# Optimization experiments

Measured on AMD Instinct MI355X. Metric: run time of the kernel, lower is better.

The kernel has to match this reference:

```python
import jax, jax.numpy as jnp
import numpy as np

N_HEAD = 16

def setup_inputs() -> dict:
    key = jax.random.key(0)
    k1, k2, k3, k4 = jax.random.split(key, 4)
    B, S, D = 4, 1024, 1024
    x = jax.random.normal(k1, (B, S, D), dtype=jnp.float32)
    # 0/1 float mask: cls_mask[:,0] overrides row 0, cls_mask[:,1] overrides col 0
    cls_mask = jax.random.randint(k2, (B, 2, S), 0, 2).astype(jnp.float32)
    w_attn = jax.random.normal(k3, (D, 3 * D), dtype=jnp.float32) * 0.02
    b_attn = jnp.zeros((3 * D,), dtype=jnp.float32)
    w_proj = jax.random.normal(k4, (D, D), dtype=jnp.float32) * 0.02
    b_proj = jnp.zeros((D,), dtype=jnp.float32)
    return {"x": x, "cls_mask": cls_mask, "w_attn": w_attn, "b_attn": b_attn,
            "w_proj": w_proj, "b_proj": b_proj}

def reference(x, cls_mask, w_attn, b_attn, w_proj, b_proj):
    B, S, D = x.shape
    H = N_HEAD
    hd = D // H
    cm = jnp.broadcast_to(jnp.tril(jnp.ones((S, S), x.dtype))[None, None], (B, 1, S, S))
    cm = cm.at[:, :, 0, :].set(cls_mask[:, 0][:, None, :])
    cm = cm.at[:, :, :, 0].set(cls_mask[:, 1][:, None, :])
    qkv = x @ w_attn + b_attn                      # [B,S,3D]
    q, k, v = jnp.split(qkv, 3, axis=-1)
    split_heads = lambda t: t.reshape(B, S, H, hd).transpose(0, 2, 1, 3)  # [B,H,S,hd]
    q, k, v = split_heads(q), split_heads(k), split_heads(v)
    w = jnp.einsum('bhqd,bhkd->bhqk', q, k) / jnp.sqrt(jnp.asarray(hd, x.dtype))
    w = w * cm - 10000.0 * (1.0 - cm)
    w = jax.nn.softmax(w, axis=-1)
    a = jnp.einsum('bhqk,bhkd->bhqd', w, v)
    a = a.transpose(0, 2, 1, 3).reshape(B, S, D)   # merge heads
    a = a @ w_proj + b_proj
    present = jnp.stack((k, v))                    # [2,B,H,S,hd]
    return a, present
```

## Files before the change

### kernel.cpp

```cpp
#include <hip/hip_runtime.h>
#include <hip/hip_bf16.h>

typedef __bf16 bf16x8 __attribute__((ext_vector_type(8)));
typedef float f32x4 __attribute__((ext_vector_type(4)));

__device__ __forceinline__ f32x4 mfma16(bf16x8 a, bf16x8 b, f32x4 c) {
    return __builtin_amdgcn_mfma_f32_16x16x32_bf16(a, b, c, 0, 0, 0);
}

typedef __attribute__((address_space(1))) const unsigned int GUInt;
typedef __attribute__((address_space(3))) unsigned int LUInt;
__device__ __forceinline__ void gl_lds16(const void* g, void* l) {
    __builtin_amdgcn_global_load_lds((GUInt*)g, (LUInt*)l, 16, 0, 0);
}

__device__ __forceinline__ int psw(int row, int bir) {
    return row * 128 + (bir ^ ((row & 7) << 4));
}

__global__ __launch_bounds__(256) void prep_kernel(
    const float* __restrict__ x, __hip_bfloat16* __restrict__ Xbf,
    const float* __restrict__ w_attn, __hip_bfloat16* __restrict__ WattnT,
    const float* __restrict__ w_proj, __hip_bfloat16* __restrict__ WprojT) {
    __shared__ float tile[64][65];
    const int bid = blockIdx.x;
    const int tid = threadIdx.x;
    if (bid < 4096) {
        int i = bid * 256 + tid;
        float4 v = reinterpret_cast<const float4*>(x)[i];
        __hip_bfloat16 o[4];
        o[0] = __float2bfloat16(v.x); o[1] = __float2bfloat16(v.y);
        o[2] = __float2bfloat16(v.z); o[3] = __float2bfloat16(v.w);
        *reinterpret_cast<uint2*>(&Xbf[i * 4]) = *reinterpret_cast<const uint2*>(o);
        return;
    }
    const float* in; __hip_bfloat16* out; int K, N, t;
    if (bid < 4096 + 768) { t = bid - 4096; in = w_attn; out = WattnT; K = 1024; N = 3072; }
    else                  { t = bid - 4864; in = w_proj; out = WprojT; K = 1024; N = 1024; }
    const int kt = t & 15, nt = t >> 4;
    const int c = tid & 63, r4 = tid >> 6;
#pragma unroll
    for (int i = 0; i < 16; ++i) {
        int r = i * 4 + r4;
        tile[r][c] = in[(size_t)(kt * 64 + r) * N + nt * 64 + c];
    }
    __syncthreads();
#pragma unroll
    for (int i = 0; i < 16; ++i) {
        int rr = i * 4 + r4;
        out[(size_t)(nt * 64 + rr) * K + kt * 64 + c] = __float2bfloat16(tile[c][rr]);
    }
}

template <int EPI>
__global__ __launch_bounds__(256) void gemm_kernel(
    const __hip_bfloat16* __restrict__ A, const __hip_bfloat16* __restrict__ Bt,
    const float* __restrict__ bias, int M, int N, int K,
    float* __restrict__ Cf,
    __hip_bfloat16* __restrict__ Qbf, __hip_bfloat16* __restrict__ Kbf,
    __hip_bfloat16* __restrict__ VbfT, float* __restrict__ present) {
    __shared__ __align__(16) char As[128 * 128];
    __shared__ __align__(16) char Bs[128 * 128];
    const int tid = threadIdx.x;
    const int lane = tid & 63;
    const int w = tid >> 6;
    const int lr = lane & 15;
    const int lg = lane >> 4;
    const int wm = (w >> 1) * 64;
    const int wn = (w & 1) * 64;
    const int bm = blockIdx.y, bn = blockIdx.x;
    const int swz = (lr & 7) << 4;

    const int srow = tid >> 3;
    const int ccs = ((tid & 7) * 16) ^ ((srow & 7) << 4);
    const char* aBase = (const char*)A + ((size_t)(bm * 128 + srow) * K) * 2 + ccs;
    const char* bBase = (const char*)Bt + ((size_t)(bn * 128 + srow) * K) * 2 + ccs;

    f32x4 zv = {0.f, 0.f, 0.f, 0.f};
    f32x4 acc[4][4];
#pragma unroll
    for (int i = 0; i < 4; ++i)
#pragma unroll
        for (int j = 0; j < 4; ++j) acc[i][j] = zv;

    for (int k0 = 0; k0 < K; k0 += 64) {
#pragma unroll
        for (int j = 0; j < 4; ++j) {
            gl_lds16(aBase + ((size_t)j * 32 * K + k0) * 2, &As[j * 4096 + tid * 16]);
            gl_lds16(bBase + ((size_t)j * 32 * K + k0) * 2, &Bs[j * 4096 + tid * 16]);
        }
        __syncthreads();
#pragma unroll
        for (int kk = 0; kk < 2; ++kk) {
            bf16x8 af[4], bfr[4];
#pragma unroll
            for (int mt = 0; mt < 4; ++mt)
                af[mt] = *reinterpret_cast<const bf16x8*>(
                    &As[(wm + mt * 16 + lr) * 128 + ((kk * 64 + lg * 16) ^ swz)]);
#pragma unroll
            for (int nt = 0; nt < 4; ++nt)
                bfr[nt] = *reinterpret_cast<const bf16x8*>(
                    &Bs[(wn + nt * 16 + lr) * 128 + ((kk * 64 + lg * 16) ^ swz)]);
#pragma unroll
            for (int mt = 0; mt < 4; ++mt)
#pragma unroll
                for (int nt = 0; nt < 4; ++nt)
                    acc[mt][nt] = mfma16(af[mt], bfr[nt], acc[mt][nt]);
        }
        __syncthreads();
    }

#pragma unroll
    for (int mt = 0; mt < 4; ++mt) {
        const int mbase = bm * 128 + wm + mt * 16 + lg * 4;
        const int bb = mbase >> 10, s0 = mbase & 1023;
#pragma unroll
        for (int nt = 0; nt < 4; ++nt) {
            const int n = bn * 128 + wn + nt * 16 + lr;
            const float bias_n = bias[n];
            float v[4];
#pragma unroll
            for (int r = 0; r < 4; ++r) v[r] = acc[mt][nt][r] + bias_n;
            if (EPI == 0) {
#pragma unroll
                for (int r = 0; r < 4; ++r) Cf[(size_t)(mbase + r) * N + n] = v[r];
            } else {
                const int sec = n >> 10, nn = n & 1023;
                const int hh = nn >> 6, d = nn & 63;
                const int rowbase = ((bb * 16 + hh) * 1024 + s0) * 64 + d;
                if (sec == 0) {
#pragma unroll
                    for (int r = 0; r < 4; ++r) Qbf[rowbase + r * 64] = __float2bfloat16(v[r]);
                } else if (sec == 1) {
#pragma unroll
                    for (int r = 0; r < 4; ++r) {
                        Kbf[rowbase + r * 64] = __float2bfloat16(v[r]);
                        present[rowbase + r * 64] = v[r];
                    }
                } else {
                    __hip_bfloat16 pk[4];
#pragma unroll
                    for (int r = 0; r < 4; ++r) {
                        pk[r] = __float2bfloat16(v[r]);
                        present[4194304 + rowbase + r * 64] = v[r];
                    }
                    *reinterpret_cast<uint2*>(&VbfT[((bb * 16 + hh) * 64 + d) * 1024 + s0]) =
                        *reinterpret_cast<const uint2*>(pk);
                }
            }
        }
    }
}

template <bool FIRST>
__device__ __forceinline__ void attn_tile(
    const char* Kb, const char* Vb, int kv0, char* Pw,
    const bf16x8* aq, const float* clscol, const float* cls, int b, int qbase,
    f32x4* acc_o, f32x4& acc_l,
    int lr, int lg, int lk, int swz, bf16x8 ones, float SC) {
    f32x4 zv = {0.f, 0.f, 0.f, 0.f};
    f32x4 sacc[4];
#pragma unroll
    for (int nt = 0; nt < 4; ++nt) {
        const char* kr = Kb + (nt * 16 + lr) * 128;
        bf16x8 k0 = *reinterpret_cast<const bf16x8*>(kr + ((lg * 16) ^ swz));
        bf16x8 k1 = *reinterpret_cast<const bf16x8*>(kr + ((64 + lg * 16) ^ swz));
        sacc[nt] = mfma16(aq[1], k1, mfma16(aq[0], k0, zv));
    }
    float p[4][4];
#pragma unroll
    for (int nt = 0; nt < 4; ++nt) {
        int k_j = kv0 + nt * 16 + lr;
#pragma unroll
        for (int r = 0; r < 4; ++r) {
            int q_i = qbase + lg * 4 + r;
            float e = __builtin_amdgcn_exp2f(sacc[nt][r] * SC);
            p[nt][r] = (k_j <= q_i) ? e : 0.f;
        }
    }
    if (qbase == 0) {
#pragma unroll
        for (int nt = 0; nt < 4; ++nt) {
            float cr = cls[b * 2048 + kv0 + nt * 16 + lr];
            float e0 = __builtin_amdgcn_exp2f(sacc[nt][0] * SC);
            float pr = (cr != 0.f) ? e0 : 0.f;
            if (lg == 0) p[nt][0] = pr;
        }
    }
    if (FIRST) {
#pragma unroll
        for (int r = 0; r < 4; ++r) {
            float ec = __builtin_amdgcn_exp2f(sacc[0][r] * SC);
            float pc = (clscol[r] != 0.f) ? ec : 0.f;
            if (lr == 0) p[0][r] = pc;
        }
    }
#pragma unroll
    for (int nt = 0; nt < 4; ++nt)
#pragma unroll
        for (int r = 0; r < 4; ++r)
            *reinterpret_cast<__hip_bfloat16*>(&Pw[psw(lg * 4 + r, nt * 32 + lr * 2)]) =
                __float2bfloat16(p[nt][r]);
    bf16x8 pa0 = *reinterpret_cast<const bf16x8*>(&Pw[psw(lr, lk * 2)]);
    bf16x8 pa1 = *reinterpret_cast<const bf16x8*>(&Pw[psw(lr, 64 + lk * 2)]);
    acc_l = mfma16(pa1, ones, mfma16(pa0, ones, acc_l));
#pragma unroll
    for (int ntd = 0; ntd < 4; ++ntd) {
        const char* vr = Vb + (ntd * 16 + lr) * 128;
        bf16x8 v0 = *reinterpret_cast<const bf16x8*>(vr + ((lg * 16) ^ swz));
        bf16x8 v1 = *reinterpret_cast<const bf16x8*>(vr + ((64 + lg * 16) ^ swz));
        acc_o[ntd] = mfma16(pa1, v1, mfma16(pa0, v0, acc_o[ntd]));
    }
}

__global__ __launch_bounds__(256) void attn_kernel(
    const __hip_bfloat16* __restrict__ Qbf, const __hip_bfloat16* __restrict__ Kbf,
    const __hip_bfloat16* __restrict__ VbfT, const float* __restrict__ cls,
    __hip_bfloat16* __restrict__ Abf) {
    __shared__ __align__(16) char KV0[16384];
    __shared__ __align__(16) char KV1[16384];
    __shared__ __align__(16) char P_lds[4 * 2048];
    const int tid = threadIdx.x;
    const int lane = tid & 63;
    const int w = tid >> 6;
    const int lr = lane & 15;
    const int lg = lane >> 4;
    const int lk = lg * 8;
    const int bh = blockIdx.x;
    const int qx = blockIdx.y;
    const int b = bh >> 4, h = bh & 15;
    const int desc[16] = {15, 0, 14, 13, 12, 11, 10, 9, 8, 7, 6, 5, 4, 3, 2, 1};
    const int base = (qx + ((b & 2) ? 8 : 0)) & 15;
    const int pos = (b & 1) ? (15 - base) : base;
    const int qt = desc[pos];
    const int qbase = qt * 64 + w * 16;
    char* Pw = &P_lds[w * 2048];
    const int ntiles = (qt == 0) ? 16 : (qt + 1);

    const char* kSrc = (const char*)Kbf + (size_t)bh * 131072;
    const char* vSrc = (const char*)VbfT + (size_t)bh * 131072;
    const int srow = tid >> 3;
    const int ccs = ((tid & 7) * 16) ^ ((srow & 7) << 4);

#define STAGE(BUFPTR, T)                                                         \
    do {                                                                         \
        const int kv0s_ = (T) * 64;                                              \
        char* dst_ = &(BUFPTR)[tid * 16];                                        \
        gl_lds16(kSrc + (size_t)(kv0s_ + srow) * 128 + ccs, dst_);               \
        gl_lds16(kSrc + (size_t)(kv0s_ + 32 + srow) * 128 + ccs, dst_ + 4096);   \
        gl_lds16(vSrc + (size_t)srow * 2048 + kv0s_ * 2 + ccs, dst_ + 8192);     \
        gl_lds16(vSrc + (size_t)(32 + srow) * 2048 + kv0s_ * 2 + ccs, dst_ + 12288); \
    } while (0)

    STAGE(KV0, 0);

    bf16x8 aq[2];
#pragma unroll
    for (int c = 0; c < 2; ++c)
        aq[c] = *reinterpret_cast<const bf16x8*>(&Qbf[(size_t)(bh * 1024 + qbase + lr) * 64 + c * 32 + lk]);

    float clscol[4];
#pragma unroll
    for (int r = 0; r < 4; ++r)
        clscol[r] = cls[b * 2048 + 1024 + qbase + lg * 4 + r];

    bf16x8 ones;
#pragma unroll
    for (int i = 0; i < 8; ++i) ones[i] = (__bf16)1.0f;

    const float SC = 0.125f * 1.44269504088896f;
    f32x4 zv = {0.f, 0.f, 0.f, 0.f};
    f32x4 acc_o[4];
    f32x4 acc_l = zv;
#pragma unroll
    for (int i = 0; i < 4; ++i) acc_o[i] = zv;

    const int swz = (lr & 7) << 4;
    __syncthreads();

    STAGE(KV1, 1);
    attn_tile<true>(KV0, KV0 + 8192, 0, Pw, aq, clscol, cls, b, qbase,
                    acc_o, acc_l, lr, lg, lk, swz, ones, SC);
    __syncthreads();
    int t = 1;
    while (t < ntiles) {
        if (t + 1 < ntiles) STAGE(KV0, t + 1);
        attn_tile<false>(KV1, KV1 + 8192, t * 64, Pw, aq, clscol, cls, b, qbase,
                         acc_o, acc_l, lr, lg, lk, swz, ones, SC);
        __syncthreads();
        ++t;
        if (t >= ntiles) break;
        if (t + 1 < ntiles) STAGE(KV1, t + 1);
        attn_tile<false>(KV0, KV0 + 8192, t * 64, Pw, aq, clscol, cls, b, qbase,
                         acc_o, acc_l, lr, lg, lk, swz, ones, SC);
        __syncthreads();
        ++t;
    }
#undef STAGE

#pragma unroll
    for (int r = 0; r < 4; ++r) {
        float inv = 1.f / acc_l[r];
        int q_i = qbase + lg * 4 + r;
#pragma unroll
        for (int ntd = 0; ntd < 4; ++ntd) {
            int dd = ntd * 16 + lr;
            Abf[(size_t)(b * 1024 + q_i) * 1024 + h * 64 + dd] = __float2bfloat16(acc_o[ntd][r] * inv);
        }
    }
}

extern "C" void kernel_launch(void* const* d_in, const int* in_sizes, int n_in,
                              void* d_out, int out_size, void* d_ws, size_t ws_size,
                              hipStream_t stream) {
    const float* x      = (const float*)d_in[0];
    const float* cls    = (const float*)d_in[1];
    const float* w_attn = (const float*)d_in[2];
    const float* b_attn = (const float*)d_in[3];
    const float* w_proj = (const float*)d_in[4];
    const float* b_proj = (const float*)d_in[5];
    float* out_a = (float*)d_out;
    float* present = out_a + 4194304;

    char* ws = (char*)d_ws;
    __hip_bfloat16* Xbf    = (__hip_bfloat16*)(ws);
    __hip_bfloat16* Abf    = (__hip_bfloat16*)(ws);
    __hip_bfloat16* WattnT = (__hip_bfloat16*)(ws + 12ull * 1024 * 1024);
    __hip_bfloat16* WprojT = (__hip_bfloat16*)(ws + 20ull * 1024 * 1024);
    __hip_bfloat16* Qbf    = (__hip_bfloat16*)(ws + 24ull * 1024 * 1024);
    __hip_bfloat16* Kbf    = (__hip_bfloat16*)(ws + 36ull * 1024 * 1024);
    __hip_bfloat16* VbfT   = (__hip_bfloat16*)(ws + 48ull * 1024 * 1024);

    prep_kernel<<<5120, 256, 0, stream>>>(x, Xbf, w_attn, WattnT, w_proj, WprojT);
    gemm_kernel<1><<<dim3(24, 32), 256, 0, stream>>>(Xbf, WattnT, b_attn, 4096, 3072, 1024,
                                                     nullptr, Qbf, Kbf, VbfT, present);
    attn_kernel<<<dim3(64, 16), 256, 0, stream>>>(Qbf, Kbf, VbfT, cls, Abf);
    gemm_kernel<0><<<dim3(8, 32), 256, 0, stream>>>(Abf, WprojT, b_proj, 4096, 1024, 1024,
                                                    out_a, nullptr, nullptr, nullptr, nullptr);
}
```

Measured before the change: 107.9 us.

## Keep attention probabilities in registers via transposed QK^T and fold scale into Q

The QK^T MFMA now runs with operands swapped, so each lane holds S^T fragments. That lets the exponentiated probabilities be packed straight into bf16x8 A-operands for the PV MFMA, dropping the per-wave P staging buffer in LDS and its scattered stores and reloads. The V loads are rearranged into 8-byte pieces to match the permuted key order. The softmax scale times log2(e) is folded into Q in the QKV GEMM epilogue, which removes a multiply per score. Scaling Q before the bf16 rounding slightly changes rounding, and the CLS row/column masking logic is remapped to the new fragment layout.

```diff
diff --git a/kernel.cpp b/kernel.cpp
--- a/kernel.cpp
+++ b/kernel.cpp
@@ -12,10 +12,6 @@
 typedef __attribute__((address_space(3))) unsigned int LUInt;
 __device__ __forceinline__ void gl_lds16(const void* g, void* l) {
     __builtin_amdgcn_global_load_lds((GUInt*)g, (LUInt*)l, 16, 0, 0);
-}
-
-__device__ __forceinline__ int psw(int row, int bir) {
-    return row * 128 + (bir ^ ((row & 7) << 4));
 }
 
 __global__ __launch_bounds__(256) void prep_kernel(
@@ -110,6 +106,7 @@
         __syncthreads();
     }
 
+    const float SCQ = 0.18033688011112f;
 #pragma unroll
     for (int mt = 0; mt < 4; ++mt) {
         const int mbase = bm * 128 + wm + mt * 16 + lg * 4;
@@ -130,7 +127,8 @@
                 const int rowbase = ((bb * 16 + hh) * 1024 + s0) * 64 + d;
                 if (sec == 0) {
 #pragma unroll
-                    for (int r = 0; r < 4; ++r) Qbf[rowbase + r * 64] = __float2bfloat16(v[r]);
+                    for (int r = 0; r < 4; ++r)
+                        Qbf[rowbase + r * 64] = __float2bfloat16(v[r] * SCQ);
                 } else if (sec == 1) {
 #pragma unroll
                     for (int r = 0; r < 4; ++r) {
@@ -154,10 +152,10 @@
 
 template <bool FIRST>
 __device__ __forceinline__ void attn_tile(
-    const char* Kb, const char* Vb, int kv0, char* Pw,
-    const bf16x8* aq, const float* clscol, const float* cls, int b, int qbase,
+    const char* Kb, const char* Vb, int kv0,
+    const bf16x8* aq, float clscolq, const float* cls, int b, int qbase,
     f32x4* acc_o, f32x4& acc_l,
-    int lr, int lg, int lk, int swz, bf16x8 ones, float SC) {
+    int lr, int lg, int swz, bf16x8 ones) {
     f32x4 zv = {0.f, 0.f, 0.f, 0.f};
     f32x4 sacc[4];
 #pragma unroll
@@ -165,51 +163,59 @@
         const char* kr = Kb + (nt * 16 + lr) * 128;
         bf16x8 k0 = *reinterpret_cast<const bf16x8*>(kr + ((lg * 16) ^ swz));
         bf16x8 k1 = *reinterpret_cast<const bf16x8*>(kr + ((64 + lg * 16) ^ swz));
-        sacc[nt] = mfma16(aq[1], k1, mfma16(aq[0], k0, zv));
+        sacc[nt] = mfma16(k1, aq[1], mfma16(k0, aq[0], zv));
     }
     float p[4][4];
+    const int q_i = qbase + lr;
 #pragma unroll
     for (int nt = 0; nt < 4; ++nt) {
-        int k_j = kv0 + nt * 16 + lr;
+        int kbase = kv0 + nt * 16 + lg * 4;
 #pragma unroll
         for (int r = 0; r < 4; ++r) {
-            int q_i = qbase + lg * 4 + r;
-            float e = __builtin_amdgcn_exp2f(sacc[nt][r] * SC);
-            p[nt][r] = (k_j <= q_i) ? e : 0.f;
+            float e = __builtin_amdgcn_exp2f(sacc[nt][r]);
+            p[nt][r] = (kbase + r <= q_i) ? e : 0.f;
         }
     }
     if (qbase == 0) {
 #pragma unroll
-        for (int nt = 0; nt < 4; ++nt) {
-            float cr = cls[b * 2048 + kv0 + nt * 16 + lr];
-            float e0 = __builtin_amdgcn_exp2f(sacc[nt][0] * SC);
-            float pr = (cr != 0.f) ? e0 : 0.f;
-            if (lg == 0) p[nt][0] = pr;
-        }
+        for (int nt = 0; nt < 4; ++nt)
+#pragma unroll
+            for (int r = 0; r < 4; ++r) {
+                float cr = cls[b * 2048 + kv0 + nt * 16 + lg * 4 + r];
+                float e = __builtin_amdgcn_exp2f(sacc[nt][r]);
+                float pr = (cr != 0.f) ? e : 0.f;
+                if (lr == 0) p[nt][r] = pr;
+            }
     }
     if (FIRST) {
+        float ec = __builtin_amdgcn_exp2f(sacc[0][0]);
+        float pc = (clscolq != 0.f) ? ec : 0.f;
+        if (lg == 0) p[0][0] = pc;
+    }
+    bf16x8 pa8[2];
+#pragma unroll
+    for (int j = 0; j < 2; ++j) {
+        bf16x8 v;
 #pragma unroll
         for (int r = 0; r < 4; ++r) {
-            float ec = __builtin_amdgcn_exp2f(sacc[0][r] * SC);
-            float pc = (clscol[r] != 0.f) ? ec : 0.f;
-            if (lr == 0) p[0][r] = pc;
-        }
-    }
-#pragma unroll
-    for (int nt = 0; nt < 4; ++nt)
-#pragma unroll
-        for (int r = 0; r < 4; ++r)
-            *reinterpret_cast<__hip_bfloat16*>(&Pw[psw(lg * 4 + r, nt * 32 + lr * 2)]) =
-                __float2bfloat16(p[nt][r]);
-    bf16x8 pa0 = *reinterpret_cast<const bf16x8*>(&Pw[psw(lr, lk * 2)]);
-    bf16x8 pa1 = *reinterpret_cast<const bf16x8*>(&Pw[psw(lr, 64 + lk * 2)]);
-    acc_l = mfma16(pa1, ones, mfma16(pa0, ones, acc_l));
+            v[r] = (__bf16)p[2 * j][r];
+            v[r + 4] = (__bf16)p[2 * j + 1][r];
+        }
+        pa8[j] = v;
+    }
+    acc_l = mfma16(pa8[1], ones, mfma16(pa8[0], ones, acc_l));
 #pragma unroll
     for (int ntd = 0; ntd < 4; ++ntd) {
         const char* vr = Vb + (ntd * 16 + lr) * 128;
-        bf16x8 v0 = *reinterpret_cast<const bf16x8*>(vr + ((lg * 16) ^ swz));
-        bf16x8 v1 = *reinterpret_cast<const bf16x8*>(vr + ((64 + lg * 16) ^ swz));
-        acc_o[ntd] = mfma16(pa1, v1, mfma16(pa0, v0, acc_o[ntd]));
+        f32x4 a = acc_o[ntd];
+#pragma unroll
+        for (int j = 0; j < 2; ++j) {
+            uint2 lo = *reinterpret_cast<const uint2*>(vr + (((2 * j) * 32 + lg * 8) ^ swz));
+            uint2 hi = *reinterpret_cast<const uint2*>(vr + (((2 * j + 1) * 32 + lg * 8) ^ swz));
+            uint4 q4 = {lo.x, lo.y, hi.x, hi.y};
+            a = mfma16(pa8[j], __builtin_bit_cast(bf16x8, q4), a);
+        }
+        acc_o[ntd] = a;
     }
 }
 
@@ -219,7 +225,6 @@
     __hip_bfloat16* __restrict__ Abf) {
     __shared__ __align__(16) char KV0[16384];
     __shared__ __align__(16) char KV1[16384];
-    __shared__ __align__(16) char P_lds[4 * 2048];
     const int tid = threadIdx.x;
     const int lane = tid & 63;
     const int w = tid >> 6;
@@ -234,7 +239,6 @@
     const int pos = (b & 1) ? (15 - base) : base;
     const int qt = desc[pos];
     const int qbase = qt * 64 + w * 16;
-    char* Pw = &P_lds[w * 2048];
     const int ntiles = (qt == 0) ? 16 : (qt + 1);
 
     const char* kSrc = (const char*)Kbf + (size_t)bh * 131072;
@@ -259,16 +263,12 @@
     for (int c = 0; c < 2; ++c)
         aq[c] = *reinterpret_cast<const bf16x8*>(&Qbf[(size_t)(bh * 1024 + qbase + lr) * 64 + c * 32 + lk]);
 
-    float clscol[4];
-#pragma unroll
-    for (int r = 0; r < 4; ++r)
-        clscol[r] = cls[b * 2048 + 1024 + qbase + lg * 4 + r];
+    const float clscolq = cls[b * 2048 + 1024 + qbase + lr];
 
     bf16x8 ones;
 #pragma unroll
     for (int i = 0; i < 8; ++i) ones[i] = (__bf16)1.0f;
 
-    const float SC = 0.125f * 1.44269504088896f;
     f32x4 zv = {0.f, 0.f, 0.f, 0.f};
     f32x4 acc_o[4];
     f32x4 acc_l = zv;
@@ -279,20 +279,20 @@
     __syncthreads();
 
     STAGE(KV1, 1);
-    attn_tile<true>(KV0, KV0 + 8192, 0, Pw, aq, clscol, cls, b, qbase,
-                    acc_o, acc_l, lr, lg, lk, swz, ones, SC);
+    attn_tile<true>(KV0, KV0 + 8192, 0, aq, clscolq, cls, b, qbase,
+                    acc_o, acc_l, lr, lg, swz, ones);
     __syncthreads();
     int t = 1;
     while (t < ntiles) {
         if (t + 1 < ntiles) STAGE(KV0, t + 1);
-        attn_tile<false>(KV1, KV1 + 8192, t * 64, Pw, aq, clscol, cls, b, qbase,
-                         acc_o, acc_l, lr, lg, lk, swz, ones, SC);
+        attn_tile<false>(KV1, KV1 + 8192, t * 64, aq, clscolq, cls, b, qbase,
+                         acc_o, acc_l, lr, lg, swz, ones);
         __syncthreads();
         ++t;
         if (t >= ntiles) break;
         if (t + 1 < ntiles) STAGE(KV1, t + 1);
-        attn_tile<false>(KV0, KV0 + 8192, t * 64, Pw, aq, clscol, cls, b, qbase,
-                         acc_o, acc_l, lr, lg, lk, swz, ones, SC);
+        attn_tile<false>(KV0, KV0 + 8192, t * 64, aq, clscolq, cls, b, qbase,
+                         acc_o, acc_l, lr, lg, swz, ones);
         __syncthreads();
         ++t;
     }
```

Measured after the change: 118.2 us. 9.6% more time.
